# Optimization experiments

Hardware: AMD Instinct MI355X
Metric: run time of the kernel (lower is better)

Reference implementation:

```python
import jax, jax.numpy as jnp
import numpy as np

B, T, D, H, L = 32, 512, 1024, 1024, 2


def setup_inputs() -> dict:
    key = jax.random.key(0)
    ks = jax.random.split(key, 8)
    s_in = 1.0 / np.sqrt(D)   # approximate orthogonal-init scale
    s_h = 1.0 / np.sqrt(H)
    return {
        "x": jax.random.normal(ks[0], (B, T, D), jnp.float32),
        "hidden": jnp.zeros((L, B, H), jnp.float32),
        "w_ih0": jax.random.normal(ks[1], (3 * H, D), jnp.float32) * s_in,
        "w_hh0": jax.random.normal(ks[2], (3 * H, H), jnp.float32) * s_h,
        "b_ih0": jnp.zeros((3 * H,), jnp.float32),
        "b_hh0": jnp.zeros((3 * H,), jnp.float32),
        "w_ih1": jax.random.normal(ks[3], (3 * H, H), jnp.float32) * s_h,
        "w_hh1": jax.random.normal(ks[4], (3 * H, H), jnp.float32) * s_h,
        "b_ih1": jnp.zeros((3 * H,), jnp.float32),
        "b_hh1": jnp.zeros((3 * H,), jnp.float32),
    }


def _gru_layer(x, h0, w_ih, w_hh, b_ih, b_hh):
    # x: [B,T,Din] -> precompute input projection once (as in source)
    xp = jnp.einsum('btd,gd->btg', x, w_ih) + b_ih        # [B,T,3H]
    xp_t = jnp.swapaxes(xp, 0, 1)                          # [T,B,3H]

    def step(h, xpt):
        hp = h @ w_hh.T + b_hh                             # [B,3H]
        r = jax.nn.sigmoid(xpt[:, :H] + hp[:, :H])
        z = jax.nn.sigmoid(xpt[:, H:2 * H] + hp[:, H:2 * H])
        n = jnp.tanh(xpt[:, 2 * H:] + r * hp[:, 2 * H:])
        h_new = (1 - z) * n + z * h
        return h_new, h_new

    h_last, ys = jax.lax.scan(step, h0, xp_t)              # ys: [T,B,H]
    return jnp.swapaxes(ys, 0, 1), h_last


def reference(x, hidden, w_ih0, w_hh0, b_ih0, b_hh0,
              w_ih1, w_hh1, b_ih1, b_hh1):
    y0, h0 = _gru_layer(x, hidden[0], w_ih0, w_hh0, b_ih0, b_hh0)
    y1, h1 = _gru_layer(y0, hidden[1], w_ih1, w_hh1, b_ih1, b_hh1)
    # dropout rates are 0.0 (eval semantics) -> identity
    return y1, jnp.stack([h0, h1], axis=0)
```

## Files before the change

### kernel.cpp

```cpp
#include <hip/hip_runtime.h>
#include <hip/hip_bf16.h>

#define NB 32
#define NT 512
#define NH 1024
#define G3 3072
#define NWG 128
#define LDS_BLOB 98304
#define LDS_PART 16384
#define LDS_HPF  8192
#define LDS_HLOC 2048
#define PK_LDS (LDS_BLOB + LDS_PART + LDS_HPF + LDS_HLOC)

typedef __attribute__((ext_vector_type(8))) short short8;
typedef __attribute__((ext_vector_type(4))) float f32x4;
typedef __attribute__((ext_vector_type(4))) unsigned short us4;
typedef unsigned long long u64;

static __device__ __forceinline__ unsigned short f2bf(float f) {
    union { float f; unsigned u; } v; v.f = f;
    if ((v.u & 0x7fffffffu) > 0x7f800000u) return (unsigned short)((v.u >> 16) | 0x0040u);
    unsigned u = v.u + 0x7fffu + ((v.u >> 16) & 1u);
    return (unsigned short)(u >> 16);
}

static __device__ __forceinline__ short8 coh_load16(const u64* p) {
    u64 lo = __hip_atomic_load(p,     __ATOMIC_RELAXED, __HIP_MEMORY_SCOPE_AGENT);
    u64 hi = __hip_atomic_load(p + 1, __ATOMIC_RELAXED, __HIP_MEMORY_SCOPE_AGENT);
    union { u64 u[2]; short8 s; } r;
    r.u[0] = lo; r.u[1] = hi;
    return r.s;
}
static __device__ __forceinline__ void coh_store8(u64* p, u64 v) {
    __hip_atomic_store(p, v, __ATOMIC_RELAXED, __HIP_MEMORY_SCOPE_AGENT);
}

__global__ __launch_bounds__(256) void cvt_bf16_v4(const float4* __restrict__ src,
                                                   us4* __restrict__ dst, int n4) {
    for (int i = blockIdx.x * 256 + threadIdx.x; i < n4; i += gridDim.x * 256) {
        float4 v = src[i];
        us4 o;
        o.x = f2bf(v.x); o.y = f2bf(v.y); o.z = f2bf(v.z); o.w = f2bf(v.w);
        dst[i] = o;
    }
}

__global__ __launch_bounds__(256) void txp_x(const float4* __restrict__ x, us4* __restrict__ xt) {
    const int total = NT * NB * 256;
    for (int i = blockIdx.x * 256 + threadIdx.x; i < total; i += gridDim.x * 256) {
        int b = i / (NT * 256);
        int rem = i - b * (NT * 256);
        int t = rem >> 8;
        int d4 = rem & 255;
        float4 v = x[i];
        us4 o;
        o.x = f2bf(v.x); o.y = f2bf(v.y); o.z = f2bf(v.z); o.w = f2bf(v.w);
        xt[((size_t)t * NB + b) * 256 + d4] = o;
    }
}

__global__ __launch_bounds__(256) void init_h(const float* __restrict__ hid,
                                              unsigned short* __restrict__ h0b,
                                              unsigned short* __restrict__ h1b) {
    int i = blockIdx.x * 256 + threadIdx.x;
    h0b[i] = f2bf(hid[i]);
    h1b[i] = f2bf(hid[NB * NH + i]);
}

__global__ __launch_bounds__(256, 1) void gru_persistent(
    const unsigned short* __restrict__ xt,
    unsigned short* __restrict__ y0b,
    const unsigned short* __restrict__ wih0, const unsigned short* __restrict__ whh0,
    const unsigned short* __restrict__ wih1, const unsigned short* __restrict__ whh1,
    const float* __restrict__ bih0, const float* __restrict__ bhh0,
    const float* __restrict__ bih1, const float* __restrict__ bhh1,
    const float* __restrict__ hid,
    unsigned short* __restrict__ hb00, unsigned short* __restrict__ hb01,
    unsigned short* __restrict__ hb10, unsigned short* __restrict__ hb11,
    float* __restrict__ out,
    int* __restrict__ flags)
{
    extern __shared__ char lds[];
    short* blob = (short*)lds;
    float* part = (float*)(lds + LDS_BLOB);
    float* hpf  = (float*)(lds + LDS_BLOB + LDS_PART);
    float* hloc = (float*)(lds + LDS_BLOB + LDS_PART + LDS_HPF);

    const int tid  = threadIdx.x;
    const int lane = tid & 63;
    const int wv   = tid >> 6;
    const int kh   = wv & 1;
    const int mt   = wv >> 1;
    const int lr   = lane & 15;
    const int lq   = lane >> 4;

    const int wg   = blockIdx.x;
    const int lay  = wg >> 6;
    const int slot = wg & 63;
    const int j0   = slot * 16;

    int* fl0   = flags;
    int* flown = lay ? (flags + 64 * 32) : flags;

    const unsigned short* wih = lay ? wih1 : wih0;
    const unsigned short* whh = lay ? whh1 : whh0;
    const float* bih = lay ? bih1 : bih0;
    const float* bhh = lay ? bhh1 : bhh0;
    unsigned short* hb[2];
    if (lay == 0) { hb[0] = hb00; hb[1] = hb01; }
    else          { hb[0] = hb10; hb[1] = hb11; }

    for (int c = tid; c < 6144; c += 256) {
        int g   = c >> 11;
        int rem = c & 2047;
        int kt  = rem >> 6;
        int q   = (rem >> 4) & 3;
        int col = rem & 15;
        *(short8*)(blob + c * 8) =
            *(const short8*)((const short*)whh + (size_t)(g * 1024 + j0 + col) * 1024 + kt * 32 + q * 8);
    }

    float br_[4], bz_[4], bxn_[4], bhn_[4];
    if (tid < 128) {
        const int b = tid >> 2, c4 = (tid & 3) * 4;
#pragma unroll
        for (int j = 0; j < 4; ++j) {
            int gc = j0 + c4 + j;
            br_[j]  = bih[gc] + bhh[gc];
            bz_[j]  = bih[1024 + gc] + bhh[1024 + gc];
            bxn_[j] = bih[2048 + gc];
            bhn_[j] = bhh[2048 + gc];
        }
        float4 h0 = *(const float4*)&hid[(size_t)lay * NB * NH + (size_t)b * 1024 + j0 + c4];
        *(float4*)&hloc[b * 16 + c4] = h0;
    }
    __syncthreads();

    const int aoff = (mt * 16 + lr) * 1024 + lq * 8;
    const short* wiB = (const short*)wih + (size_t)(j0 + lr) * 1024 + lq * 8;

    for (int t = 0; t < NT; ++t) {
        if (lay == 1) {
            if (wv == 0) {
                const int* p = fl0 + lane * 32;
                while (__hip_atomic_load(p, __ATOMIC_RELAXED, __HIP_MEMORY_SCOPE_AGENT) < t + 1)
                    __builtin_amdgcn_s_sleep(1);
            }
            asm volatile("" ::: "memory");
            __syncthreads();
        }

        f32x4 acc0 = {0.f,0.f,0.f,0.f};
        f32x4 acc1 = {0.f,0.f,0.f,0.f};
        f32x4 acc2 = {0.f,0.f,0.f,0.f};
        f32x4 acc3 = {0.f,0.f,0.f,0.f};

        if (lay == 0) {
            const short* Ap = (const short*)xt + (size_t)t * NB * 1024 + aoff;
#pragma unroll 8
            for (int kk = 0; kk < 16; ++kk) {
                const int kt = kh * 16 + kk;
                short8 a  = *(const short8*)(Ap + kt * 32);
                short8 b0 = *(const short8*)(wiB + kt * 32);
                short8 b1 = *(const short8*)(wiB + 1024 * 1024 + kt * 32);
                short8 b2 = *(const short8*)(wiB + 2 * 1024 * 1024 + kt * 32);
                acc0 = __builtin_amdgcn_mfma_f32_16x16x32_bf16(a, b0, acc0, 0, 0, 0);
                acc1 = __builtin_amdgcn_mfma_f32_16x16x32_bf16(a, b1, acc1, 0, 0, 0);
                acc2 = __builtin_amdgcn_mfma_f32_16x16x32_bf16(a, b2, acc2, 0, 0, 0);
            }
        } else {
            const u64* Ap = (const u64*)((const short*)y0b + (size_t)t * NB * 1024 + aoff);
#pragma unroll 8
            for (int kk = 0; kk < 16; ++kk) {
                const int kt = kh * 16 + kk;
                short8 a  = coh_load16(Ap + kt * 8);
                short8 b0 = *(const short8*)(wiB + kt * 32);
                short8 b1 = *(const short8*)(wiB + 1024 * 1024 + kt * 32);
                short8 b2 = *(const short8*)(wiB + 2 * 1024 * 1024 + kt * 32);
                acc0 = __builtin_amdgcn_mfma_f32_16x16x32_bf16(a, b0, acc0, 0, 0, 0);
                acc1 = __builtin_amdgcn_mfma_f32_16x16x32_bf16(a, b1, acc1, 0, 0, 0);
                acc2 = __builtin_amdgcn_mfma_f32_16x16x32_bf16(a, b2, acc2, 0, 0, 0);
            }
        }

        if (wv == 0) {
            const int* p = flown + lane * 32;
            while (__hip_atomic_load(p, __ATOMIC_RELAXED, __HIP_MEMORY_SCOPE_AGENT) < t)
                __builtin_amdgcn_s_sleep(1);
        }
        asm volatile("" ::: "memory");
        __syncthreads();

        {
            const u64* Hb = (const u64*)((const short*)hb[t & 1] + aoff);
#pragma unroll 8
            for (int kk = 0; kk < 16; ++kk) {
                const int kt = kh * 16 + kk;
                short8 a  = coh_load16(Hb + kt * 8);
                short8 c0 = *(const short8*)(blob + kt * 512 + lane * 8);
                short8 c1 = *(const short8*)(blob + (32 + kt) * 512 + lane * 8);
                short8 c2 = *(const short8*)(blob + (64 + kt) * 512 + lane * 8);
                acc0 = __builtin_amdgcn_mfma_f32_16x16x32_bf16(a, c0, acc0, 0, 0, 0);
                acc1 = __builtin_amdgcn_mfma_f32_16x16x32_bf16(a, c1, acc1, 0, 0, 0);
                acc3 = __builtin_amdgcn_mfma_f32_16x16x32_bf16(a, c2, acc3, 0, 0, 0);
            }
        }

        *(f32x4*)(part + ((wv * 4 + 0) * 64 + lane) * 4) = acc0;
        *(f32x4*)(part + ((wv * 4 + 1) * 64 + lane) * 4) = acc1;
        *(f32x4*)(part + ((wv * 4 + 2) * 64 + lane) * 4) = acc2;
        *(f32x4*)(part + ((wv * 4 + 3) * 64 + lane) * 4) = acc3;
        __syncthreads();

        for (int eo = tid; eo < 2048; eo += 256) {
            int g2 = eo >> 9, b = (eo >> 4) & 31, c = eo & 15;
            int m = b >> 4, r = b & 3, l = ((b >> 2) & 3) * 16 + c;
            float v = part[(((m * 2 + 0) * 4 + g2) * 64 + l) * 4 + r]
                    + part[(((m * 2 + 1) * 4 + g2) * 64 + l) * 4 + r];
            hpf[eo] = v;
        }
        __syncthreads();

        if (tid < 128) {
            const int b = tid >> 2, c4 = (tid & 3) * 4;
            const int gc0 = j0 + c4;
            float hn[4];
            u64 hpack = 0;
#pragma unroll
            for (int j = 0; j < 4; ++j) {
                const int e = b * 16 + c4 + j;
                float pr  = hpf[e];
                float pz  = hpf[512 + e];
                float pxn = hpf[1024 + e];
                float phn = hpf[1536 + e];
                float r = 1.f / (1.f + __expf(-(pr + br_[j])));
                float z = 1.f / (1.f + __expf(-(pz + bz_[j])));
                float n = tanhf(pxn + bxn_[j] + r * (phn + bhn_[j]));
                float hprev = hloc[e];
                float h = (1.f - z) * n + z * hprev;
                hloc[e] = h;
                hn[j] = h;
                hpack |= (u64)f2bf(h) << (16 * j);
            }
            coh_store8((u64*)((unsigned short*)hb[(t + 1) & 1] + (size_t)b * 1024 + gc0), hpack);
            if (lay == 0) {
                coh_store8((u64*)(y0b + ((size_t)t * NB + b) * 1024 + gc0), hpack);
            } else {
                float4 o4; o4.x = hn[0]; o4.y = hn[1]; o4.z = hn[2]; o4.w = hn[3];
                *(float4*)&out[((size_t)b * NT + t) * 1024 + gc0] = o4;
            }
            if (t == NT - 1) {
                float4 o4; o4.x = hn[0]; o4.y = hn[1]; o4.z = hn[2]; o4.w = hn[3];
                *(float4*)&out[(size_t)NB * NT * 1024 + (size_t)lay * NB * NH + (size_t)b * 1024 + gc0] = o4;
            }
        }

        asm volatile("s_waitcnt vmcnt(0)" ::: "memory");
        __syncthreads();
        if (tid == 0)
            __hip_atomic_store(flown + slot * 32, t + 1, __ATOMIC_RELAXED, __HIP_MEMORY_SCOPE_AGENT);
    }
}

extern "C" void kernel_launch(void* const* d_in, const int* in_sizes, int n_in,
                              void* d_out, int out_size, void* d_ws, size_t ws_size,
                              hipStream_t stream) {
    (void)in_sizes; (void)n_in; (void)out_size; (void)ws_size;

    const float* x     = (const float*)d_in[0];
    const float* hid   = (const float*)d_in[1];
    const float* w_ih0 = (const float*)d_in[2];
    const float* w_hh0 = (const float*)d_in[3];
    const float* b_ih0 = (const float*)d_in[4];
    const float* b_hh0 = (const float*)d_in[5];
    const float* w_ih1 = (const float*)d_in[6];
    const float* w_hh1 = (const float*)d_in[7];
    const float* b_ih1 = (const float*)d_in[8];
    const float* b_hh1 = (const float*)d_in[9];
    float* out = (float*)d_out;

    char* ws = (char*)d_ws;
    size_t off = 0;
    auto alloc = [&](size_t bytes) -> void* {
        void* p = ws + off;
        off += (bytes + 255) & ~(size_t)255;
        return p;
    };

    unsigned short* xtb   = (unsigned short*)alloc((size_t)NT * NB * 1024 * 2);
    unsigned short* y0b   = (unsigned short*)alloc((size_t)NT * NB * 1024 * 2);
    unsigned short* wih0b = (unsigned short*)alloc((size_t)G3 * 1024 * 2);
    unsigned short* whh0b = (unsigned short*)alloc((size_t)G3 * 1024 * 2);
    unsigned short* wih1b = (unsigned short*)alloc((size_t)G3 * 1024 * 2);
    unsigned short* whh1b = (unsigned short*)alloc((size_t)G3 * 1024 * 2);
    unsigned short* hb0[2]; unsigned short* hb1[2];
    for (int i = 0; i < 2; i++) hb0[i] = (unsigned short*)alloc(NB * NH * 2);
    for (int i = 0; i < 2; i++) hb1[i] = (unsigned short*)alloc(NB * NH * 2);
    int* flags = (int*)alloc(2 * 64 * 32 * sizeof(int));

    txp_x<<<2048, 256, 0, stream>>>((const float4*)x, (us4*)xtb);
    cvt_bf16_v4<<<512, 256, 0, stream>>>((const float4*)w_ih0, (us4*)wih0b, G3 * 1024 / 4);
    cvt_bf16_v4<<<512, 256, 0, stream>>>((const float4*)w_hh0, (us4*)whh0b, G3 * 1024 / 4);
    cvt_bf16_v4<<<512, 256, 0, stream>>>((const float4*)w_ih1, (us4*)wih1b, G3 * 1024 / 4);
    cvt_bf16_v4<<<512, 256, 0, stream>>>((const float4*)w_hh1, (us4*)whh1b, G3 * 1024 / 4);
    init_h<<<NB * NH / 256, 256, 0, stream>>>(hid, hb0[0], hb1[0]);
    hipMemsetAsync(flags, 0, 2 * 64 * 32 * sizeof(int), stream);

    (void)hipFuncSetAttribute((const void*)gru_persistent,
                              hipFuncAttributeMaxDynamicSharedMemorySize, PK_LDS);
    gru_persistent<<<NWG, 256, PK_LDS, stream>>>(
        xtb, y0b, wih0b, whh0b, wih1b, whh1b,
        b_ih0, b_hh0, b_ih1, b_hh1, hid,
        hb0[0], hb0[1], hb1[0], hb1[1],
        out, flags);
}
```

Baseline: 8.378 ms.

## Replace workgroup-wide flag barriers with per-wave batch-half flags and fast tanh

Cross-workgroup synchronization is made finer-grained. Each of the two batch halves (mt) gets its own publish flag per slot, written by the wave that finished that half. Every wave now polls only the 64 flags for its batch rows, with no workgroup barrier, instead of wave 0 polling and then a __syncthreads. The aim is to shorten the serial critical path of each recurrent timestep. It also swaps tanhf for an exp-based formula, which risks overflow or NaN for large negative arguments and changes the memory-ordering assumptions.

```diff
diff --git a/kernel.cpp b/kernel.cpp
--- a/kernel.cpp
+++ b/kernel.cpp
@@ -99,8 +99,9 @@
     const int slot = wg & 63;
     const int j0   = slot * 16;
 
-    int* fl0   = flags;
-    int* flown = lay ? (flags + 64 * 32) : flags;
+    const int* poll_own = flags + lay * 128 + mt * 64 + lane;
+    const int* poll_y0  = flags + mt * 64 + lane;
+    int* pub = flags + lay * 128 + (tid >> 6) * 64 + slot;
 
     const unsigned short* wih = lay ? wih1 : wih0;
     const unsigned short* whh = lay ? whh1 : whh0;
@@ -140,16 +141,6 @@
     const short* wiB = (const short*)wih + (size_t)(j0 + lr) * 1024 + lq * 8;
 
     for (int t = 0; t < NT; ++t) {
-        if (lay == 1) {
-            if (wv == 0) {
-                const int* p = fl0 + lane * 32;
-                while (__hip_atomic_load(p, __ATOMIC_RELAXED, __HIP_MEMORY_SCOPE_AGENT) < t + 1)
-                    __builtin_amdgcn_s_sleep(1);
-            }
-            asm volatile("" ::: "memory");
-            __syncthreads();
-        }
-
         f32x4 acc0 = {0.f,0.f,0.f,0.f};
         f32x4 acc1 = {0.f,0.f,0.f,0.f};
         f32x4 acc2 = {0.f,0.f,0.f,0.f};
@@ -169,6 +160,9 @@
                 acc2 = __builtin_amdgcn_mfma_f32_16x16x32_bf16(a, b2, acc2, 0, 0, 0);
             }
         } else {
+            while (__hip_atomic_load(poll_y0, __ATOMIC_RELAXED, __HIP_MEMORY_SCOPE_AGENT) < t + 1)
+                __builtin_amdgcn_s_sleep(1);
+            asm volatile("" ::: "memory");
             const u64* Ap = (const u64*)((const short*)y0b + (size_t)t * NB * 1024 + aoff);
 #pragma unroll 8
             for (int kk = 0; kk < 16; ++kk) {
@@ -183,13 +177,9 @@
             }
         }
 
-        if (wv == 0) {
-            const int* p = flown + lane * 32;
-            while (__hip_atomic_load(p, __ATOMIC_RELAXED, __HIP_MEMORY_SCOPE_AGENT) < t)
-                __builtin_amdgcn_s_sleep(1);
-        }
+        while (__hip_atomic_load(poll_own, __ATOMIC_RELAXED, __HIP_MEMORY_SCOPE_AGENT) < t)
+            __builtin_amdgcn_s_sleep(1);
         asm volatile("" ::: "memory");
-        __syncthreads();
 
         {
             const u64* Hb = (const u64*)((const short*)hb[t & 1] + aoff);
@@ -235,7 +225,9 @@
                 float phn = hpf[1536 + e];
                 float r = 1.f / (1.f + __expf(-(pr + br_[j])));
                 float z = 1.f / (1.f + __expf(-(pz + bz_[j])));
-                float n = tanhf(pxn + bxn_[j] + r * (phn + bhn_[j]));
+                float na = pxn + bxn_[j] + r * (phn + bhn_[j]);
+                float e2 = __expf(-2.f * na);
+                float n = (1.f - e2) / (1.f + e2);
                 float hprev = hloc[e];
                 float h = (1.f - z) * n + z * hprev;
                 hloc[e] = h;
@@ -243,9 +235,14 @@
                 hpack |= (u64)f2bf(h) << (16 * j);
             }
             coh_store8((u64*)((unsigned short*)hb[(t + 1) & 1] + (size_t)b * 1024 + gc0), hpack);
-            if (lay == 0) {
+            if (lay == 0)
                 coh_store8((u64*)(y0b + ((size_t)t * NB + b) * 1024 + gc0), hpack);
-            } else {
+
+            asm volatile("s_waitcnt vmcnt(0)" ::: "memory");
+            if ((tid & 63) == 0)
+                __hip_atomic_store(pub, t + 1, __ATOMIC_RELAXED, __HIP_MEMORY_SCOPE_AGENT);
+
+            if (lay == 1) {
                 float4 o4; o4.x = hn[0]; o4.y = hn[1]; o4.z = hn[2]; o4.w = hn[3];
                 *(float4*)&out[((size_t)b * NT + t) * 1024 + gc0] = o4;
             }
@@ -254,11 +251,6 @@
                 *(float4*)&out[(size_t)NB * NT * 1024 + (size_t)lay * NB * NH + (size_t)b * 1024 + gc0] = o4;
             }
         }
-
-        asm volatile("s_waitcnt vmcnt(0)" ::: "memory");
-        __syncthreads();
-        if (tid == 0)
-            __hip_atomic_store(flown + slot * 32, t + 1, __ATOMIC_RELAXED, __HIP_MEMORY_SCOPE_AGENT);
     }
 }
 
@@ -296,7 +288,7 @@
     unsigned short* hb0[2]; unsigned short* hb1[2];
     for (int i = 0; i < 2; i++) hb0[i] = (unsigned short*)alloc(NB * NH * 2);
     for (int i = 0; i < 2; i++) hb1[i] = (unsigned short*)alloc(NB * NH * 2);
-    int* flags = (int*)alloc(2 * 64 * 32 * sizeof(int));
+    int* flags = (int*)alloc(2 * 2 * 64 * sizeof(int));
 
     txp_x<<<2048, 256, 0, stream>>>((const float4*)x, (us4*)xtb);
     cvt_bf16_v4<<<512, 256, 0, stream>>>((const float4*)w_ih0, (us4*)wih0b, G3 * 1024 / 4);
@@ -304,7 +296,7 @@
     cvt_bf16_v4<<<512, 256, 0, stream>>>((const float4*)w_ih1, (us4*)wih1b, G3 * 1024 / 4);
     cvt_bf16_v4<<<512, 256, 0, stream>>>((const float4*)w_hh1, (us4*)whh1b, G3 * 1024 / 4);
     init_h<<<NB * NH / 256, 256, 0, stream>>>(hid, hb0[0], hb1[0]);
-    hipMemsetAsync(flags, 0, 2 * 64 * 32 * sizeof(int), stream);
+    hipMemsetAsync(flags, 0, 2 * 2 * 64 * sizeof(int), stream);
 
     (void)hipFuncSetAttribute((const void*)gru_persistent,
                               hipFuncAttributeMaxDynamicSharedMemorySize, PK_LDS);
```

New measurement: 7.769 ms. -7.3%, faster.
